# Kernel tuning notes

Hardware: AMD Instinct MI355X
Metric: run time of the kernel (lower is better)

Reference implementation:

```python
import jax, jax.numpy as jnp
import numpy as np

B, S, D, H, F = 4, 2048, 1024, 16, 4096
HD = D // H
NEG = -2.0 ** 32
EPS = 1e-5


def _gelu(x):
    return x * 0.5 * (1.0 + jax.scipy.special.erf(x / jnp.sqrt(2.0).astype(x.dtype)))


def _layernorm(x, scale, offset):
    mu = jnp.mean(x, axis=-1, keepdims=True)
    var = jnp.mean(jnp.square(x - mu), axis=-1, keepdims=True)
    return (x - mu) * jax.lax.rsqrt(var + EPS) * scale + offset


def setup_inputs() -> dict:
    key = jax.random.key(0)
    ks = jax.random.split(key, 12)
    s = 0.02
    return {
        "x": jax.random.normal(ks[0], (B, S, D), jnp.float32),
        "mask": jnp.zeros((B, S), jnp.int32),  # 1 = masked-out (padding)
        "Wq": jax.random.normal(ks[1], (D, D), jnp.float32) * s,
        "bq": jnp.zeros((D,), jnp.float32),
        "Wk": jax.random.normal(ks[2], (D, D), jnp.float32) * s,
        "bk": jnp.zeros((D,), jnp.float32),
        "Wv": jax.random.normal(ks[3], (D, D), jnp.float32) * s,
        "bv": jnp.zeros((D,), jnp.float32),
        "Wo": jax.random.normal(ks[4], (D, D), jnp.float32) * s,
        "bo": jnp.zeros((D,), jnp.float32),
        "ln1_s": jnp.ones((D,), jnp.float32),
        "ln1_b": jnp.zeros((D,), jnp.float32),
        "W1": jax.random.normal(ks[5], (D, F), jnp.float32) * s,
        "b1": jnp.zeros((F,), jnp.float32),
        "W2": jax.random.normal(ks[6], (F, D), jnp.float32) * s,
        "b2": jnp.zeros((D,), jnp.float32),
        "ln2_s": jnp.ones((D,), jnp.float32),
        "ln2_b": jnp.zeros((D,), jnp.float32),
    }


def reference(x, mask, Wq, bq, Wk, bk, Wv, bv, Wo, bo, ln1_s, ln1_b,
              W1, b1, W2, b2, ln2_s, ln2_b):
    b, s, d = x.shape
    q = (x @ Wq + bq).reshape(b, s, H, HD)
    k = (x @ Wk + bk).reshape(b, s, H, HD)
    v = (x @ Wv + bv).reshape(b, s, H, HD)
    logits = jnp.einsum('btnh,bsnh->bnts', q, k) / jnp.sqrt(jnp.float32(HD))
    logits = logits + (mask.astype(jnp.float32) * NEG)[:, None, None, :]
    attn = jax.nn.softmax(logits, axis=-1)
    ctx = jnp.einsum('bsnh,bnts->btnh', v, attn).reshape(b, s, d)
    attn_out = ctx @ Wo + bo
    h = _layernorm(attn_out + x, ln1_s, ln1_b)
    mlp = _gelu(h @ W1 + b1) @ W2 + b2
    return _layernorm(mlp + h, ln2_s, ln2_b)
```

## Files before the change

kernel.cpp:

```cpp
#include <hip/hip_runtime.h>
#include <hip/hip_bf16.h>

typedef __attribute__((ext_vector_type(8))) short short8;
typedef __attribute__((ext_vector_type(4))) short s16x4;
typedef __attribute__((ext_vector_type(4))) float f32x4;
typedef unsigned short u16;

#define DEV __device__ __forceinline__
#define MFMA32(a, b, c) __builtin_amdgcn_mfma_f32_16x16x32_bf16(a, b, c, 0, 0, 0)
#define MFMA16(a, b, c) __builtin_amdgcn_mfma_f32_16x16x16bf16_1k(a, b, c, 0, 0, 0)
#define SBAR() asm volatile("s_barrier" ::: "memory")

DEV u16 f2b(float f) {
    __hip_bfloat16 h = __float2bfloat16(f);
    return __builtin_bit_cast(unsigned short, h);
}

DEV float max3f(float a, float b, float c) {
    float d;
    asm("v_max3_f32 %0, %1, %2, %3" : "=v"(d) : "v"(a), "v"(b), "v"(c));
    return d;
}

DEV void gl_lds16(const u16* g, u16* l) {
    __builtin_amdgcn_global_load_lds((const unsigned int*)g, (unsigned int*)l, 16, 0, 0);
}

__global__ __launch_bounds__(256) void cast_bf16(const float* __restrict__ in, u16* __restrict__ out, int n) {
    int i = (blockIdx.x * 256 + threadIdx.x) * 4;
    if (i < n) {
        float4 v = *(const float4*)(in + i);
        ushort4 o;
        o.x = f2b(v.x); o.y = f2b(v.y); o.z = f2b(v.z); o.w = f2b(v.w);
        *(ushort4*)(out + i) = o;
    }
}

__global__ __launch_bounds__(256) void transpose_cast(const float* __restrict__ in, u16* __restrict__ out,
                                                      int R, int C) {
    __shared__ float t[32][33];
    int bx = blockIdx.x * 32;
    int by = blockIdx.y * 32;
    int tx = threadIdx.x, ty = threadIdx.y;
#pragma unroll
    for (int i = 0; i < 32; i += 8) t[ty + i][tx] = in[(size_t)(by + ty + i) * C + bx + tx];
    __syncthreads();
#pragma unroll
    for (int i = 0; i < 32; i += 8) out[(size_t)(bx + ty + i) * R + by + tx] = f2b(t[tx][ty + i]);
}

__global__ __launch_bounds__(256) void pack_bias(const float* __restrict__ bq, const float* __restrict__ bk,
                                                 const float* __restrict__ bv, const float* __restrict__ bo,
                                                 const float* __restrict__ b1, const float* __restrict__ b2,
                                                 float* __restrict__ out) {
    int i = blockIdx.x * 256 + threadIdx.x;
    if (i >= 9216) return;
    float v;
    if (i < 1024) v = bq[i];
    else if (i < 2048) v = bk[i - 1024];
    else if (i < 3072) v = bv[i - 2048];
    else if (i < 4096) v = bo[i - 3072];
    else if (i < 8192) v = b1[i - 4096];
    else v = b2[i - 8192];
    out[i] = v;
}

template <bool GELU, bool BF16OUT, bool RESID>
__global__ __launch_bounds__(256) void gemm_bt(const u16* __restrict__ A, const u16* __restrict__ B,
                                               const float* __restrict__ bias, float* __restrict__ cf,
                                               u16* __restrict__ cb, const float* __restrict__ res,
                                               int M, int N, int K) {
    __shared__ __align__(16) u16 As[128 * 32];
    __shared__ __align__(16) u16 Bs[128 * 32];
    const int tid = threadIdx.x;
    const int wid = tid >> 6, lane = tid & 63;
    const int wr = wid >> 1, wc = wid & 1;
    const int m0 = blockIdx.x * 128, n0 = blockIdx.y * 128;
    const int r16 = lane & 15, g = lane >> 4;
    const int lrow = lane >> 2, lk = (lane & 3) * 8;

    f32x4 acc[4][4];
#pragma unroll
    for (int i = 0; i < 4; i++)
#pragma unroll
        for (int j = 0; j < 4; j++) acc[i][j] = (f32x4){0.f, 0.f, 0.f, 0.f};

    const u16* ga = A + (size_t)(m0 + wid * 32 + lrow) * K + lk;
    const u16* gb = B + (size_t)(n0 + wid * 32 + lrow) * K + lk;
    u16* lA0 = &As[(wid * 32) * 32];
    u16* lA1 = &As[(wid * 32 + 16) * 32];
    u16* lB0 = &Bs[(wid * 32) * 32];
    u16* lB1 = &Bs[(wid * 32 + 16) * 32];

    for (int kt = 0; kt < K; kt += 32) {
        gl_lds16(ga + kt, lA0);
        gl_lds16(ga + (size_t)16 * K + kt, lA1);
        gl_lds16(gb + kt, lB0);
        gl_lds16(gb + (size_t)16 * K + kt, lB1);
        __syncthreads();
        short8 af[4], bfr[4];
#pragma unroll
        for (int i = 0; i < 4; i++) af[i] = *(const short8*)&As[(wr * 64 + i * 16 + r16) * 32 + g * 8];
#pragma unroll
        for (int j = 0; j < 4; j++) bfr[j] = *(const short8*)&Bs[(wc * 64 + j * 16 + r16) * 32 + g * 8];
#pragma unroll
        for (int i = 0; i < 4; i++)
#pragma unroll
            for (int j = 0; j < 4; j++) acc[i][j] = MFMA32(af[i], bfr[j], acc[i][j]);
        __syncthreads();
    }

#pragma unroll
    for (int i = 0; i < 4; i++) {
#pragma unroll
        for (int j = 0; j < 4; j++) {
#pragma unroll
            for (int r = 0; r < 4; r++) {
                int row = m0 + wr * 64 + i * 16 + g * 4 + r;
                int col = n0 + wc * 64 + j * 16 + r16;
                float v = acc[i][j][r] + bias[col];
                if (RESID) v += res[(size_t)row * N + col];
                if (GELU) v = 0.5f * v * (1.0f + erff(v * 0.70710678118654752f));
                if (BF16OUT) cb[(size_t)row * N + col] = f2b(v);
                else cf[(size_t)row * N + col] = v;
            }
        }
    }
}

__global__ __launch_bounds__(256) void attn_kernel(const u16* __restrict__ qkv, const int* __restrict__ mask,
                                                   u16* __restrict__ ctx) {
    const int tid = threadIdx.x, wid = tid >> 6, lane = tid & 63;
    const int r16 = lane & 15, g = lane >> 4;
    const int h = blockIdx.y, b = blockIdx.z;
    const size_t baserow = (size_t)b * 2048;
    const int q0 = blockIdx.x * 64;

    __shared__ __align__(16) u16 Ks[2][64 * 64];
    __shared__ __align__(16) u16 Vs[2][64 * 64];
    __shared__ __align__(16) float mb_all[2048];

    const float SCALE = 0.18033688011112042f;
    const float MNEG = -6.196328018e9f;
    const s16x4 ONES = {(short)0x3F80, (short)0x3F80, (short)0x3F80, (short)0x3F80};

    short8 qf0, qf1;
    {
        const u16* qp = qkv + (baserow + q0 + wid * 16 + r16) * 3072 + h * 64 + g * 8;
        qf0 = *(const short8*)qp;
        qf1 = *(const short8*)(qp + 32);
    }

    const int L = lane;
    const int kchunk = (L & 7) ^ (L >> 3);
    const u16* kg0 = qkv + (baserow + wid * 16 + (L >> 3)) * 3072 + 1024 + h * 64 + kchunk * 8;
    const u16* kg1 = kg0 + (size_t)8 * 3072;
    const u16* vg0 = qkv + (baserow + wid * 16 + ((L & 31) >> 1)) * 3072 + 2048 + h * 64
                     + ((L >> 5) * 16 + (L & 1) * 8);
    const u16* vg1 = vg0 + 32;
    const unsigned vaddr = (unsigned)(unsigned long long)&Vs[0][0] + (unsigned)(r16 * 2 + g * 128);

    for (int i = tid; i < 2048; i += 256) mb_all[i] = mask[baserow + i] ? MNEG : 0.0f;

    gl_lds16(kg0, &Ks[0][wid * 1024]);
    gl_lds16(kg1, &Ks[0][wid * 1024 + 512]);
    gl_lds16(vg0, &Vs[0][wid * 1024]);
    gl_lds16(vg1, &Vs[0][wid * 1024 + 512]);
    __syncthreads();

    f32x4 Ot[4];
#pragma unroll
    for (int dt = 0; dt < 4; dt++) Ot[dt] = (f32x4){0.f, 0.f, 0.f, 0.f};
    f32x4 Osum = (f32x4){0.f, 0.f, 0.f, 0.f};
    float mrun = -1e30f;

    for (int t = 0; t < 32; ++t) {
        const int cur = t & 1, nb = cur ^ 1;
        if (t < 31) {
            const size_t go = (size_t)(t + 1) * 64 * 3072;
            gl_lds16(kg0 + go, &Ks[nb][wid * 1024]);
            gl_lds16(kg1 + go, &Ks[nb][wid * 1024 + 512]);
            gl_lds16(vg0 + go, &Vs[nb][wid * 1024]);
            gl_lds16(vg1 + go, &Vs[nb][wid * 1024 + 512]);
            asm volatile("s_waitcnt vmcnt(4)" ::: "memory");
        } else {
            asm volatile("s_waitcnt vmcnt(0)" ::: "memory");
        }
        SBAR();

        f32x4 z[4];
        __builtin_amdgcn_s_setprio(1);
#pragma unroll
        for (int tt = 0; tt < 4; tt++) {
            const int row = tt * 16 + r16;
            const int swz = row & 7;
            short8 a0 = *(const short8*)&Ks[cur][row * 64 + ((g ^ swz) * 8)];
            short8 a1 = *(const short8*)&Ks[cur][row * 64 + (((4 + g) ^ swz) * 8)];
            f32x4 zz = (f32x4){0.f, 0.f, 0.f, 0.f};
            zz = MFMA32(a0, qf0, zz);
            zz = MFMA32(a1, qf1, zz);
            z[tt] = zz;
        }
        __builtin_amdgcn_s_setprio(0);

        f32x4 sv[4];
#pragma unroll
        for (int tt = 0; tt < 4; tt++) {
            f32x4 mbv = *(const f32x4*)&mb_all[t * 64 + tt * 16 + g * 4];
            sv[tt] = z[tt] * SCALE + mbv;
        }

        float m0 = max3f(sv[0][0], sv[0][1], sv[0][2]);
        float m1 = max3f(sv[0][3], sv[1][0], sv[1][1]);
        float m2 = max3f(sv[1][2], sv[1][3], sv[2][0]);
        float m3 = max3f(sv[2][1], sv[2][2], sv[2][3]);
        float m4 = max3f(sv[3][0], sv[3][1], sv[3][2]);
        float pmax = fmaxf(max3f(m0, m1, m2), max3f(m3, m4, sv[3][3]));
        pmax = fmaxf(pmax, __shfl_xor(pmax, 16));
        pmax = fmaxf(pmax, __shfl_xor(pmax, 32));

        if (!__all(pmax - mrun <= 11.5f)) {
            float mnew = fmaxf(mrun, pmax);
            float alpha = exp2f(mrun - mnew);
            mrun = mnew;
            Osum *= alpha;
#pragma unroll
            for (int dt = 0; dt < 4; dt++) Ot[dt] *= alpha;
        }

        s16x4 pb[4];
#pragma unroll
        for (int tt = 0; tt < 4; tt++) {
            f32x4 d = sv[tt] - mrun;
            float p0 = exp2f(d[0]), p1 = exp2f(d[1]), p2 = exp2f(d[2]), p3 = exp2f(d[3]);
            unsigned lo, hi;
            asm("v_cvt_pk_bf16_f32 %0, %1, %2" : "=v"(lo) : "v"(p0), "v"(p1));
            asm("v_cvt_pk_bf16_f32 %0, %1, %2" : "=v"(hi) : "v"(p2), "v"(p3));
            uint2 u; u.x = lo; u.y = hi;
            pb[tt] = __builtin_bit_cast(s16x4, u);
        }

        s16x4 vf[4][4];
        const unsigned va_cur = vaddr + (unsigned)(cur * 8192);
#pragma unroll
        for (int tt = 0; tt < 4; tt++)
#pragma unroll
            for (int dt = 0; dt < 4; dt++)
                asm volatile("ds_read_b64_tr_b16 %0, %1"
                             : "=v"(vf[tt][dt])
                             : "v"(va_cur + (unsigned)((tt * 4 + dt) * 512)));
        asm volatile("s_waitcnt lgkmcnt(0)" ::: "memory");
        __builtin_amdgcn_sched_barrier(0);
        __builtin_amdgcn_s_setprio(1);
#pragma unroll
        for (int tt = 0; tt < 4; tt++) {
#pragma unroll
            for (int dt = 0; dt < 4; dt++) Ot[dt] = MFMA16(vf[tt][dt], pb[tt], Ot[dt]);
            Osum = MFMA16(ONES, pb[tt], Osum);
        }
        __builtin_amdgcn_s_setprio(0);
        SBAR();
    }

    const float rl = 1.0f / Osum[0];
    u16* cp = ctx + (baserow + q0 + wid * 16 + r16) * 1024 + h * 64 + g * 4;
#pragma unroll
    for (int dt = 0; dt < 4; dt++) {
        ushort4 o4;
        o4.x = f2b(Ot[dt][0] * rl);
        o4.y = f2b(Ot[dt][1] * rl);
        o4.z = f2b(Ot[dt][2] * rl);
        o4.w = f2b(Ot[dt][3] * rl);
        *(ushort4*)(cp + dt * 16) = o4;
    }
}

__global__ __launch_bounds__(256) void ln_kernel(const float* __restrict__ a, const float* __restrict__ res,
                                                 const float* __restrict__ gamma, const float* __restrict__ beta,
                                                 float* __restrict__ outf, u16* __restrict__ outb) {
    const int row = blockIdx.x, tid = threadIdx.x;
    const size_t base = (size_t)row * 1024 + tid * 4;
    float4 va = *(const float4*)(a + base);
    float x0 = va.x, x1 = va.y, x2 = va.z, x3 = va.w;
    if (res) {
        float4 vr = *(const float4*)(res + base);
        x0 += vr.x; x1 += vr.y; x2 += vr.z; x3 += vr.w;
    }
    float s = x0 + x1 + x2 + x3;
    float ss = x0 * x0 + x1 * x1 + x2 * x2 + x3 * x3;
#pragma unroll
    for (int m = 1; m < 64; m <<= 1) { s += __shfl_xor(s, m, 64); ss += __shfl_xor(ss, m, 64); }
    __shared__ float red[8];
    if ((tid & 63) == 0) { red[tid >> 6] = s; red[4 + (tid >> 6)] = ss; }
    __syncthreads();
    s = red[0] + red[1] + red[2] + red[3];
    ss = red[4] + red[5] + red[6] + red[7];
    float mu = s * (1.0f / 1024.0f);
    float var = ss * (1.0f / 1024.0f) - mu * mu;
    float rstd = rsqrtf(var + 1e-5f);
    float4 g4 = *(const float4*)(gamma + tid * 4);
    float4 b4 = *(const float4*)(beta + tid * 4);
    float y0 = (x0 - mu) * rstd * g4.x + b4.x;
    float y1 = (x1 - mu) * rstd * g4.y + b4.y;
    float y2 = (x2 - mu) * rstd * g4.z + b4.z;
    float y3 = (x3 - mu) * rstd * g4.w + b4.w;
    *(float4*)(outf + base) = make_float4(y0, y1, y2, y3);
    if (outb) {
        ushort4 ob;
        ob.x = f2b(y0); ob.y = f2b(y1); ob.z = f2b(y2); ob.w = f2b(y3);
        *(ushort4*)(outb + base) = ob;
    }
}

extern "C" void kernel_launch(void* const* d_in, const int* in_sizes, int n_in, void* d_out, int out_size,
                              void* d_ws, size_t ws_size, hipStream_t stream) {
    const float* x = (const float*)d_in[0];
    const int* mask = (const int*)d_in[1];
    const float* Wq = (const float*)d_in[2];
    const float* bq = (const float*)d_in[3];
    const float* Wk = (const float*)d_in[4];
    const float* bk = (const float*)d_in[5];
    const float* Wv = (const float*)d_in[6];
    const float* bv = (const float*)d_in[7];
    const float* Wo = (const float*)d_in[8];
    const float* bo = (const float*)d_in[9];
    const float* ln1s = (const float*)d_in[10];
    const float* ln1b = (const float*)d_in[11];
    const float* W1 = (const float*)d_in[12];
    const float* b1 = (const float*)d_in[13];
    const float* W2 = (const float*)d_in[14];
    const float* b2 = (const float*)d_in[15];
    const float* ln2s = (const float*)d_in[16];
    const float* ln2b = (const float*)d_in[17];
    float* out = (float*)d_out;
    char* ws = (char*)d_ws;

    const size_t MB = 1024 * 1024;
    u16* XB = (u16*)(ws + 0);
    u16* WTq = (u16*)(ws + 16 * MB);
    u16* WTk = WTq + 1024 * 1024;
    u16* WTv = WTk + 1024 * 1024;
    u16* WTo = WTv + 1024 * 1024;
    u16* WT1 = WTo + 1024 * 1024;
    u16* WT2 = WT1 + 4096 * 1024;
    float* BIAS = (float*)(ws + 40 * MB);
    u16* QKV = (u16*)(ws + 41 * MB);
    u16* CTX = (u16*)(ws + 0);
    float* ATT = (float*)(ws + 41 * MB);
    float* Hbuf = (float*)(ws + 73 * MB);
    u16* HB = (u16*)(ws + 105 * MB);
    u16* MLP1 = (u16*)(ws + 121 * MB);
    float* MLP2 = (float*)(ws + 41 * MB);

    dim3 tb(32, 8);
    cast_bf16<<<8192, 256, 0, stream>>>(x, XB, 8192 * 1024);
    transpose_cast<<<dim3(32, 32), tb, 0, stream>>>(Wq, WTq, 1024, 1024);
    transpose_cast<<<dim3(32, 32), tb, 0, stream>>>(Wk, WTk, 1024, 1024);
    transpose_cast<<<dim3(32, 32), tb, 0, stream>>>(Wv, WTv, 1024, 1024);
    transpose_cast<<<dim3(32, 32), tb, 0, stream>>>(Wo, WTo, 1024, 1024);
    transpose_cast<<<dim3(128, 32), tb, 0, stream>>>(W1, WT1, 1024, 4096);
    transpose_cast<<<dim3(32, 128), tb, 0, stream>>>(W2, WT2, 4096, 1024);
    pack_bias<<<36, 256, 0, stream>>>(bq, bk, bv, bo, b1, b2, BIAS);

    gemm_bt<false, true, false><<<dim3(64, 24), 256, 0, stream>>>(XB, WTq, BIAS, nullptr, QKV, nullptr, 8192, 3072, 1024);
    attn_kernel<<<dim3(32, 16, 4), 256, 0, stream>>>(QKV, mask, CTX);
    gemm_bt<false, false, true><<<dim3(64, 8), 256, 0, stream>>>(CTX, WTo, BIAS + 3072, ATT, nullptr, x, 8192, 1024, 1024);
    ln_kernel<<<8192, 256, 0, stream>>>(ATT, nullptr, ln1s, ln1b, Hbuf, HB);
    gemm_bt<true, true, false><<<dim3(64, 32), 256, 0, stream>>>(HB, WT1, BIAS + 4096, nullptr, MLP1, nullptr, 8192, 4096, 1024);
    gemm_bt<false, false, true><<<dim3(64, 8), 256, 0, stream>>>(MLP1, WT2, BIAS + 8192, MLP2, nullptr, Hbuf, 8192, 1024, 4096);
    ln_kernel<<<8192, 256, 0, stream>>>(MLP2, nullptr, ln2s, ln2b, out, nullptr);
}
```

Baseline: 533.8 us.

## Single-buffer attention K/V tiles and skip mask bias for unmasked tiles

The attention kernel drops the double-buffered K/V LDS tiles and the per-block 2048-entry float mask-bias array. It instead builds a 32-bit per-tile flag word from ballots over the mask and applies the mask bias only in tiles that contain masked keys, using a fused fma for scale plus max subtraction elsewhere. This cuts LDS footprint, which may raise occupancy, and removes per-tile mask loads and adds. The cost is that global-to-LDS loads are no longer prefetched one tile ahead, so load latency is exposed before each tile behind a full __syncthreads.

```diff
diff --git a/kernel.cpp b/kernel.cpp
--- a/kernel.cpp
+++ b/kernel.cpp
@@ -9,7 +9,6 @@
 #define DEV __device__ __forceinline__
 #define MFMA32(a, b, c) __builtin_amdgcn_mfma_f32_16x16x32_bf16(a, b, c, 0, 0, 0)
 #define MFMA16(a, b, c) __builtin_amdgcn_mfma_f32_16x16x16bf16_1k(a, b, c, 0, 0, 0)
-#define SBAR() asm volatile("s_barrier" ::: "memory")
 
 DEV u16 f2b(float f) {
     __hip_bfloat16 h = __float2bfloat16(f);
@@ -136,9 +135,9 @@
     const size_t baserow = (size_t)b * 2048;
     const int q0 = blockIdx.x * 64;
 
-    __shared__ __align__(16) u16 Ks[2][64 * 64];
-    __shared__ __align__(16) u16 Vs[2][64 * 64];
-    __shared__ __align__(16) float mb_all[2048];
+    __shared__ __align__(16) u16 Ks[64 * 64];
+    __shared__ __align__(16) u16 Vs[64 * 64];
+    __shared__ unsigned tflags_sh;
 
     const float SCALE = 0.18033688011112042f;
     const float MNEG = -6.196328018e9f;
@@ -151,22 +150,29 @@
         qf1 = *(const short8*)(qp + 32);
     }
 
+    if (tid == 0) tflags_sh = 0;
+    __syncthreads();
+    for (int r = 0; r < 8; ++r) {
+        int v = mask[baserow + r * 256 + tid];
+        unsigned long long bal = __ballot(v != 0);
+        if (bal != 0 && lane == 0) atomicOr(&tflags_sh, 1u << (r * 4 + wid));
+    }
+
     const int L = lane;
     const int kchunk = (L & 7) ^ (L >> 3);
     const u16* kg0 = qkv + (baserow + wid * 16 + (L >> 3)) * 3072 + 1024 + h * 64 + kchunk * 8;
     const u16* kg1 = kg0 + (size_t)8 * 3072;
+    u16* kl0 = &Ks[wid * 1024];
+    u16* kl1 = &Ks[wid * 1024 + 512];
     const u16* vg0 = qkv + (baserow + wid * 16 + ((L & 31) >> 1)) * 3072 + 2048 + h * 64
                      + ((L >> 5) * 16 + (L & 1) * 8);
     const u16* vg1 = vg0 + 32;
-    const unsigned vaddr = (unsigned)(unsigned long long)&Vs[0][0] + (unsigned)(r16 * 2 + g * 128);
-
-    for (int i = tid; i < 2048; i += 256) mb_all[i] = mask[baserow + i] ? MNEG : 0.0f;
-
-    gl_lds16(kg0, &Ks[0][wid * 1024]);
-    gl_lds16(kg1, &Ks[0][wid * 1024 + 512]);
-    gl_lds16(vg0, &Vs[0][wid * 1024]);
-    gl_lds16(vg1, &Vs[0][wid * 1024 + 512]);
+    u16* vl0 = &Vs[wid * 1024];
+    u16* vl1 = &Vs[wid * 1024 + 512];
+    const unsigned vaddr = (unsigned)(unsigned long long)&Vs[0] + (unsigned)(r16 * 2 + g * 128);
+
     __syncthreads();
+    const unsigned tfl = tflags_sh;
 
     f32x4 Ot[4];
 #pragma unroll
@@ -175,18 +181,13 @@
     float mrun = -1e30f;
 
     for (int t = 0; t < 32; ++t) {
-        const int cur = t & 1, nb = cur ^ 1;
-        if (t < 31) {
-            const size_t go = (size_t)(t + 1) * 64 * 3072;
-            gl_lds16(kg0 + go, &Ks[nb][wid * 1024]);
-            gl_lds16(kg1 + go, &Ks[nb][wid * 1024 + 512]);
-            gl_lds16(vg0 + go, &Vs[nb][wid * 1024]);
-            gl_lds16(vg1 + go, &Vs[nb][wid * 1024 + 512]);
-            asm volatile("s_waitcnt vmcnt(4)" ::: "memory");
-        } else {
-            asm volatile("s_waitcnt vmcnt(0)" ::: "memory");
-        }
-        SBAR();
+        const int kt = t * 64;
+        const size_t go = (size_t)kt * 3072;
+        gl_lds16(kg0 + go, kl0);
+        gl_lds16(kg1 + go, kl1);
+        gl_lds16(vg0 + go, vl0);
+        gl_lds16(vg1 + go, vl1);
+        __syncthreads();
 
         f32x4 z[4];
         __builtin_amdgcn_s_setprio(1);
@@ -194,8 +195,8 @@
         for (int tt = 0; tt < 4; tt++) {
             const int row = tt * 16 + r16;
             const int swz = row & 7;
-            short8 a0 = *(const short8*)&Ks[cur][row * 64 + ((g ^ swz) * 8)];
-            short8 a1 = *(const short8*)&Ks[cur][row * 64 + (((4 + g) ^ swz) * 8)];
+            short8 a0 = *(const short8*)&Ks[row * 64 + ((g ^ swz) * 8)];
+            short8 a1 = *(const short8*)&Ks[row * 64 + (((4 + g) ^ swz) * 8)];
             f32x4 zz = (f32x4){0.f, 0.f, 0.f, 0.f};
             zz = MFMA32(a0, qf0, zz);
             zz = MFMA32(a1, qf1, zz);
@@ -203,21 +204,15 @@
         }
         __builtin_amdgcn_s_setprio(0);
 
-        f32x4 sv[4];
-#pragma unroll
-        for (int tt = 0; tt < 4; tt++) {
-            f32x4 mbv = *(const f32x4*)&mb_all[t * 64 + tt * 16 + g * 4];
-            sv[tt] = z[tt] * SCALE + mbv;
-        }
-
-        float m0 = max3f(sv[0][0], sv[0][1], sv[0][2]);
-        float m1 = max3f(sv[0][3], sv[1][0], sv[1][1]);
-        float m2 = max3f(sv[1][2], sv[1][3], sv[2][0]);
-        float m3 = max3f(sv[2][1], sv[2][2], sv[2][3]);
-        float m4 = max3f(sv[3][0], sv[3][1], sv[3][2]);
-        float pmax = fmaxf(max3f(m0, m1, m2), max3f(m3, m4, sv[3][3]));
-        pmax = fmaxf(pmax, __shfl_xor(pmax, 16));
-        pmax = fmaxf(pmax, __shfl_xor(pmax, 32));
+        float m0 = max3f(z[0][0], z[0][1], z[0][2]);
+        float m1 = max3f(z[0][3], z[1][0], z[1][1]);
+        float m2 = max3f(z[1][2], z[1][3], z[2][0]);
+        float m3 = max3f(z[2][1], z[2][2], z[2][3]);
+        float m4 = max3f(z[3][0], z[3][1], z[3][2]);
+        float zmax = fmaxf(max3f(m0, m1, m2), max3f(m3, m4, z[3][3]));
+        zmax = fmaxf(zmax, __shfl_xor(zmax, 16));
+        zmax = fmaxf(zmax, __shfl_xor(zmax, 32));
+        float pmax = zmax * SCALE;
 
         if (!__all(pmax - mrun <= 11.5f)) {
             float mnew = fmaxf(mrun, pmax);
@@ -229,26 +224,46 @@
         }
 
         s16x4 pb[4];
-#pragma unroll
-        for (int tt = 0; tt < 4; tt++) {
-            f32x4 d = sv[tt] - mrun;
-            float p0 = exp2f(d[0]), p1 = exp2f(d[1]), p2 = exp2f(d[2]), p3 = exp2f(d[3]);
-            unsigned lo, hi;
-            asm("v_cvt_pk_bf16_f32 %0, %1, %2" : "=v"(lo) : "v"(p0), "v"(p1));
-            asm("v_cvt_pk_bf16_f32 %0, %1, %2" : "=v"(hi) : "v"(p2), "v"(p3));
-            uint2 u; u.x = lo; u.y = hi;
-            pb[tt] = __builtin_bit_cast(s16x4, u);
+        const float negm = -mrun;
+        if (__builtin_expect((tfl >> t) & 1u, 0)) {
+            const int* mrow = mask + baserow + kt;
+#pragma unroll
+            for (int tt = 0; tt < 4; tt++) {
+                float p[4];
+#pragma unroll
+                for (int j = 0; j < 4; j++) {
+                    float mbj = mrow[tt * 16 + g * 4 + j] ? MNEG : 0.0f;
+                    p[j] = exp2f(__builtin_fmaf(z[tt][j], SCALE, mbj + negm));
+                }
+                unsigned lo, hi;
+                asm("v_cvt_pk_bf16_f32 %0, %1, %2" : "=v"(lo) : "v"(p[0]), "v"(p[1]));
+                asm("v_cvt_pk_bf16_f32 %0, %1, %2" : "=v"(hi) : "v"(p[2]), "v"(p[3]));
+                uint2 u; u.x = lo; u.y = hi;
+                pb[tt] = __builtin_bit_cast(s16x4, u);
+            }
+        } else {
+#pragma unroll
+            for (int tt = 0; tt < 4; tt++) {
+                float p0 = exp2f(__builtin_fmaf(z[tt][0], SCALE, negm));
+                float p1 = exp2f(__builtin_fmaf(z[tt][1], SCALE, negm));
+                float p2 = exp2f(__builtin_fmaf(z[tt][2], SCALE, negm));
+                float p3 = exp2f(__builtin_fmaf(z[tt][3], SCALE, negm));
+                unsigned lo, hi;
+                asm("v_cvt_pk_bf16_f32 %0, %1, %2" : "=v"(lo) : "v"(p0), "v"(p1));
+                asm("v_cvt_pk_bf16_f32 %0, %1, %2" : "=v"(hi) : "v"(p2), "v"(p3));
+                uint2 u; u.x = lo; u.y = hi;
+                pb[tt] = __builtin_bit_cast(s16x4, u);
+            }
         }
 
         s16x4 vf[4][4];
-        const unsigned va_cur = vaddr + (unsigned)(cur * 8192);
 #pragma unroll
         for (int tt = 0; tt < 4; tt++)
 #pragma unroll
             for (int dt = 0; dt < 4; dt++)
                 asm volatile("ds_read_b64_tr_b16 %0, %1"
                              : "=v"(vf[tt][dt])
-                             : "v"(va_cur + (unsigned)((tt * 4 + dt) * 512)));
+                             : "v"(vaddr + (unsigned)((tt * 4 + dt) * 512)));
         asm volatile("s_waitcnt lgkmcnt(0)" ::: "memory");
         __builtin_amdgcn_sched_barrier(0);
         __builtin_amdgcn_s_setprio(1);
@@ -259,7 +274,7 @@
             Osum = MFMA16(ONES, pb[tt], Osum);
         }
         __builtin_amdgcn_s_setprio(0);
-        SBAR();
+        __syncthreads();
     }
 
     const float rl = 1.0f / Osum[0];
```

Result: faster. 519.4 us (-2.7%).
